# Kernel tuning notes

Measured on AMD Instinct MI355X. Metric: run time of the kernel, lower is better.

Reference implementation:

```python
import jax, jax.numpy as jnp
import numpy as np

H = 64            # hidden_channels
L = 2             # num_layers
E = 300_000       # edges per relation
B = 64            # graphs in batch
NS = [100_000, 20_000, 50_000, 80_000]   # variable, value, operator, constraint
# (src_type, dst_type) for the 9 hetero relations, fixed order
RELS = [(0,1),(0,2),(0,3),(2,3),(3,3),(1,0),(2,0),(3,0),(3,2)]
R = len(RELS)
SLOPE = 0.2       # GATConv leaky_relu negative slope


def setup_inputs() -> dict:
    key = jax.random.key(0)
    ks = iter(jax.random.split(key, 64))
    inp = {}
    for n, N in zip(["x_variable", "x_value", "x_operator", "x_constraint"], NS):
        inp[n] = jax.random.normal(next(ks), (N, H), jnp.float32)
    sc = 1.0 / np.sqrt(H).astype(np.float32)
    inp["Wsrc"] = jax.random.normal(next(ks), (L, R, H, H), jnp.float32) * sc
    inp["Wdst"] = jax.random.normal(next(ks), (L, R, H, H), jnp.float32) * sc
    inp["asrc"] = jax.random.normal(next(ks), (L, R, H), jnp.float32) * sc
    inp["adst"] = jax.random.normal(next(ks), (L, R, H), jnp.float32) * sc
    inp["bias"] = jax.random.normal(next(ks), (L, R, H), jnp.float32) * 0.01
    inp["lin_w"] = jax.random.normal(next(ks), (2, 2 * H), jnp.float32) / np.sqrt(2.0 * H).astype(np.float32)
    inp["lin_b"] = jnp.zeros((2,), jnp.float32)
    for r, (s, d) in enumerate(RELS):
        inp[f"src{r}"] = jax.random.randint(next(ks), (E,), 0, NS[s], jnp.int32)
        inp[f"dst{r}"] = jax.random.randint(next(ks), (E,), 0, NS[d], jnp.int32)
    inp["batch_variable"] = jnp.sort(jax.random.randint(next(ks), (NS[0],), 0, B, jnp.int32))
    inp["batch_constraint"] = jnp.sort(jax.random.randint(next(ks), (NS[3],), 0, B, jnp.int32))
    inp["num_graphs"] = B
    return inp


def _gat(xs, xd, Ws, Wd, a_s, a_d, b, src, dst):
    """Bipartite PyG GATConv (heads=1, add_self_loops=False)."""
    hs = xs @ Ws                         # [Ns, H]
    hd = xd @ Wd                         # [Nd, H]
    al_s = hs @ a_s                      # [Ns]
    al_d = hd @ a_d                      # [Nd]
    score = jax.nn.leaky_relu(al_s[src] + al_d[dst], SLOPE)    # [E]
    nd = xd.shape[0]
    m = jax.ops.segment_max(score, dst, num_segments=nd)
    p = jnp.exp(score - m[dst])
    z = jax.ops.segment_sum(p, dst, num_segments=nd)
    alpha = p / (z[dst] + 1e-16)                               # segment softmax
    out = jax.ops.segment_sum(hs[src] * alpha[:, None], dst, num_segments=nd)
    return out + b


def _seg_mean(x, seg, n):
    s = jax.ops.segment_sum(x, seg, num_segments=n)
    c = jax.ops.segment_sum(jnp.ones((x.shape[0],), x.dtype), seg, num_segments=n)
    return s / jnp.maximum(c, 1.0)[:, None]


def reference(x_variable, x_value, x_operator, x_constraint,
              Wsrc, Wdst, asrc, adst, bias, lin_w, lin_b,
              src0, dst0, src1, dst1, src2, dst2, src3, dst3, src4, dst4,
              src5, dst5, src6, dst6, src7, dst7, src8, dst8,
              batch_variable, batch_constraint, num_graphs):
    xs = [x_variable, x_value, x_operator, x_constraint]
    srcs = [src0, src1, src2, src3, src4, src5, src6, src7, src8]
    dsts = [dst0, dst1, dst2, dst3, dst4, dst5, dst6, dst7, dst8]
    for l in range(L):
        out = [jnp.zeros((x.shape[0], H), x.dtype) for x in xs]
        for r, (s, d) in enumerate(RELS):
            out[d] = out[d] + _gat(xs[s], xs[d], Wsrc[l, r], Wdst[l, r],
                                   asrc[l, r], adst[l, r], bias[l, r],
                                   srcs[r], dsts[r])
        xs = [jax.nn.relu(o) for o in out]   # dropout is identity in eval
    vp = _seg_mean(xs[0], batch_variable, num_graphs)   # [B, H]
    cp = _seg_mean(xs[3], batch_constraint, num_graphs) # [B, H]
    return jnp.concatenate([vp, cp], axis=1) @ lin_w.T + lin_b   # [B, 2]
```

## Files before the change

### kernel.cpp

```cpp
#include <hip/hip_runtime.h>
#include <hip/hip_bf16.h>

#define NH 64
#define NRELS 9
#define NEDGE 300000
#define NGRAPH 64
#define TOTROWS 250000
#define TOTFSEG 660000
#define TOTEDGE (NRELS * NEDGE)
#define NBUCK 977
#define NBC 4
#define CHUNK 2048
#define NBLK ((TOTEDGE + CHUNK - 1) / CHUNK)
#define KCH 20
#define KSP 66
#define BKT_CAP 6144

typedef __attribute__((ext_vector_type(8))) short short8;
typedef __attribute__((ext_vector_type(4))) float f32x4;

__constant__ int c_NS[4]     = {100000, 20000, 50000, 80000};
__constant__ int c_SRC[9]    = {0,0,0,2,3,1,2,3,3};
__constant__ int c_DST[9]    = {1,2,3,3,3,0,0,0,2};
__constant__ int c_XOFF[5]   = {0,100000,120000,170000,250000};
__constant__ int c_ASOFF[10] = {0,100000,200000,300000,350000,430000,450000,500000,580000,660000};
__constant__ int c_FOFF[5]   = {0,300000,320000,420000,660000};
__constant__ int c_NRELT[4]  = {3,1,2,3};
__constant__ int c_RRANK[9]  = {0,0,0,1,2,0,1,2,1};

struct EdgePtrs { const int* s[9]; const int* d[9]; };

__device__ __forceinline__ unsigned short f2bf(float f) {
  union { __hip_bfloat16 h; unsigned short u; } c;
  c.h = __float2bfloat16(f);
  return c.u;
}

__device__ __forceinline__ float wred_max32(float v) {
#pragma unroll
  for (int o = 16; o; o >>= 1) v = fmaxf(v, __shfl_xor(v, o, 32));
  return v;
}

__global__ void k_setup(const float* Wsrc, const float* Wdst, const float* asrc,
                        const float* adst, const float* bias, float* wv, float* bsum) {
  int b = blockIdx.x, j = threadIdx.x;
  if (b < 36) {
    int r = b % 9, q = b / 9;
    int l = q >> 1, side = q & 1;
    const float* W = (side ? Wdst : Wsrc) + (l * 9 + r) * 64 * 64;
    const float* a = (side ? adst : asrc) + (l * 9 + r) * 64;
    float s = 0.f;
    for (int i = 0; i < 64; ++i) s += W[j * 64 + i] * a[i];
    wv[(side ? 1152 : 0) + (l * 9 + r) * 64 + j] = s;
  } else {
    for (int l = 0; l < 2; ++l)
      for (int t = 0; t < 4; ++t) {
        float s = 0.f;
        for (int r = 0; r < 9; ++r)
          if (c_DST[r] == t) s += bias[(l * 9 + r) * 64 + j];
        bsum[(l * 4 + t) * 64 + j] = s;
      }
  }
}

__global__ __launch_bounds__(256) void k_bhist2(EdgePtrs Eg, int* bh) {
  __shared__ int sh[NBUCK];
  for (int i = threadIdx.x; i < NBUCK; i += 256) sh[i] = 0;
  __syncthreads();
  int lo = blockIdx.x * CHUNK;
  int hi = lo + CHUNK; if (hi > TOTEDGE) hi = TOTEDGE;
  for (int gid = lo + threadIdx.x; gid < hi; gid += 256) {
    int r = gid / NEDGE, e = gid - r * NEDGE;
    int g = c_XOFF[c_DST[r]] + Eg.d[r][e];
    atomicAdd(&sh[g >> 8], 1);
  }
  __syncthreads();
  int* dst = bh + (size_t)blockIdx.x * NBUCK;
  for (int i = threadIdx.x; i < NBUCK; i += 256) dst[i] = sh[i];
}

__global__ void k_cs1(const int* bh, int* csum) {
  int blk = blockIdx.x;
  int c = blk / NBC;
  int b = (blk % NBC) * 256 + threadIdx.x;
  if (b >= NBUCK) return;
  int k0 = c * KSP;
  int k1 = k0 + KSP; if (k1 > NBLK) k1 = NBLK;
  int s = 0;
  for (int k = k0; k < k1; ++k) s += bh[(size_t)k * NBUCK + b];
  csum[(size_t)c * NBUCK + b] = s;
}

__global__ void k_cs2(int* csum, int* gbh) {
  int b = blockIdx.x * 256 + threadIdx.x;
  if (b >= NBUCK) return;
  int run = 0;
#pragma unroll
  for (int c = 0; c < KCH; ++c) {
    size_t idx = (size_t)c * NBUCK + b;
    int t = csum[idx];
    csum[idx] = run;
    run += t;
  }
  gbh[b] = run;
}

__global__ void k_cs3(int* bh, const int* csum) {
  int blk = blockIdx.x;
  int c = blk / NBC;
  int b = (blk % NBC) * 256 + threadIdx.x;
  if (b >= NBUCK) return;
  int k0 = c * KSP;
  int k1 = k0 + KSP; if (k1 > NBLK) k1 = NBLK;
  int run = csum[(size_t)c * NBUCK + b];
  for (int k = k0; k < k1; ++k) {
    size_t idx = (size_t)k * NBUCK + b;
    int t = bh[idx];
    bh[idx] = run;
    run += t;
  }
}

__global__ void k_bscan(const int* gbh, int* boff) {
  __shared__ int sd[1024];
  int t = threadIdx.x;
  int v = (t < NBUCK) ? gbh[t] : 0;
  sd[t] = v; __syncthreads();
  for (int o = 1; o < 1024; o <<= 1) {
    int x = (t >= o) ? sd[t - o] : 0; __syncthreads();
    sd[t] += x; __syncthreads();
  }
  if (t < NBUCK) boff[t] = sd[t] - v;
  if (t == 1023) boff[NBUCK] = sd[1023];
}

__global__ __launch_bounds__(256) void k_bin2(EdgePtrs Eg, const int* bh, const int* boff, int* pairs) {
  __shared__ int cur[NBUCK];
  const int* mybh = bh + (size_t)blockIdx.x * NBUCK;
  for (int i = threadIdx.x; i < NBUCK; i += 256) cur[i] = boff[i] + mybh[i];
  __syncthreads();
  int lo = blockIdx.x * CHUNK;
  int hi = lo + CHUNK; if (hi > TOTEDGE) hi = TOTEDGE;
  for (int gid = lo + threadIdx.x; gid < hi; gid += 256) {
    int r = gid / NEDGE, e = gid - r * NEDGE;
    int g = c_XOFF[c_DST[r]] + Eg.d[r][e];
    int b = g >> 8;
    int pos = atomicAdd(&cur[b], 1);
    int key = ((g & 255) << 2) | c_RRANK[r];
    pairs[pos] = (key << 20) | (c_ASOFF[r] + Eg.s[r][e]);
  }
}

__global__ __launch_bounds__(256) void k_bsort(const int* pairs, const int* boff,
                                               int* rowptr, int* asx) {
  __shared__ int spl[BKT_CAP];
  __shared__ int sout[BKT_CAP];
  __shared__ int ssc[1024];
  __shared__ int scur[1024];
  __shared__ int sws[256];
  int b = blockIdx.x, t = threadIdx.x;
  int lo = boff[b], hi = boff[b + 1];
  int n = hi - lo; if (n > BKT_CAP) n = BKT_CAP;
  for (int i = t; i < n; i += 256) spl[i] = pairs[lo + i];
  for (int i = t; i < 1024; i += 256) ssc[i] = 0;
  __syncthreads();
  for (int i = t; i < n; i += 256) atomicAdd(&ssc[((unsigned)spl[i]) >> 20], 1);
  __syncthreads();
  int c0 = ssc[t * 4], c1 = ssc[t * 4 + 1], c2 = ssc[t * 4 + 2], c3 = ssc[t * 4 + 3];
  int s = c0 + c1 + c2 + c3;
  sws[t] = s;
  __syncthreads();
  for (int o = 1; o < 256; o <<= 1) {
    int x = (t >= o) ? sws[t - o] : 0; __syncthreads();
    sws[t] += x; __syncthreads();
  }
  int base = sws[t] - s;
  ssc[t * 4]     = base;
  ssc[t * 4 + 1] = base + c0;
  ssc[t * 4 + 2] = base + c0 + c1;
  ssc[t * 4 + 3] = base + c0 + c1 + c2;
  scur[t * 4]     = ssc[t * 4];
  scur[t * 4 + 1] = ssc[t * 4 + 1];
  scur[t * 4 + 2] = ssc[t * 4 + 2];
  scur[t * 4 + 3] = ssc[t * 4 + 3];
  __syncthreads();
  int nodeBase = b << 8;
  for (int i = t; i < 1024; i += 256) {
    int l = i >> 2, rank = i & 3;
    int g = nodeBase + l;
    if (g < TOTROWS) {
      int tt = (g >= c_XOFF[1]) + (g >= c_XOFF[2]) + (g >= c_XOFF[3]);
      int nr = c_NRELT[tt];
      if (rank < nr)
        rowptr[c_FOFF[tt] + (g - c_XOFF[tt]) * nr + rank] = lo + ssc[i];
    }
  }
  if (b == 0 && t == 0) rowptr[TOTFSEG] = TOTEDGE;
  for (int i = t; i < n; i += 256) {
    int p = spl[i];
    int pos = atomicAdd(&scur[((unsigned)p) >> 20], 1);
    sout[pos] = (int)(((((unsigned)p >> 20) & 3u) << 20) | ((unsigned)p & 0xFFFFFu));
  }
  __syncthreads();
  for (int i = t; i < n; i += 256) asx[lo + i] = sout[i];
}

struct AlphaP {
  const float* x0; const float* x1; const float* x2; const float* x3;
  float* als; float* ald;
  const float* wvs; const float* wvd;
  int act; int smask; int dmask;
};

__global__ __launch_bounds__(256) void k_alphas(AlphaP P) {
  __shared__ float sws[576];
  __shared__ float swd[576];
  for (int i = threadIdx.x; i < 576; i += 256) { sws[i] = P.wvs[i]; swd[i] = P.wvd[i]; }
  __syncthreads();
  int node = blockIdx.x * 256 + threadIdx.x;
  if (node >= TOTROWS) return;
  int t = (node >= c_XOFF[1]) + (node >= c_XOFF[2]) + (node >= c_XOFF[3]);
  int n = node - c_XOFF[t];
  const float* xt = t == 0 ? P.x0 : t == 1 ? P.x1 : t == 2 ? P.x2 : P.x3;
  const float4* rp = (const float4*)xt + (size_t)n * 16;
  float4 row[16];
#pragma unroll
  for (int k = 0; k < 16; ++k) row[k] = rp[k];
  if (P.act) {
#pragma unroll
    for (int k = 0; k < 16; ++k) {
      row[k].x = fmaxf(row[k].x, 0.f); row[k].y = fmaxf(row[k].y, 0.f);
      row[k].z = fmaxf(row[k].z, 0.f); row[k].w = fmaxf(row[k].w, 0.f);
    }
  }
#pragma unroll
  for (int r = 0; r < 9; ++r) {
    bool ns = ((P.smask >> r) & 1) && (c_SRC[r] == t);
    bool nd = ((P.dmask >> r) & 1) && (c_DST[r] == t);
    if (ns) {
      float s = 0.f;
#pragma unroll
      for (int k = 0; k < 16; ++k) {
        float4 w = *(const float4*)&sws[r * 64 + k * 4];
        s += row[k].x * w.x + row[k].y * w.y + row[k].z * w.z + row[k].w * w.w;
      }
      P.als[c_ASOFF[r] + n] = s;
    }
    if (nd) {
      float s = 0.f;
#pragma unroll
      for (int k = 0; k < 16; ++k) {
        float4 w = *(const float4*)&swd[r * 64 + k * 4];
        s += row[k].x * w.x + row[k].y * w.y + row[k].z * w.z + row[k].w * w.w;
      }
      P.ald[c_FOFF[t] + n * c_NRELT[t] + c_RRANK[r]] = s;
    }
  }
}

struct GemmAllP {
  const float* x0; const float* x1; const float* x2; const float* x3;
  const float* Wl;
  __hip_bfloat16* hs;
  int act; int ntyp;
  int tbase[5];
  int typ[4];
  int nrel[4];
  int rel[4][3];
};

#define XSTR 72

__global__ __launch_bounds__(256) void k_gemma(GemmAllP G) {
  __shared__ unsigned short sx[64 * XSTR];
  __shared__ unsigned short sw[64 * XSTR];
  int bid = blockIdx.x;
  int k = 0;
#pragma unroll 3
  for (int q = 1; q < 4; ++q) if (q < G.ntyp) k += (bid >= G.tbase[q]);
  int st = G.typ[k];
  int tile = bid - G.tbase[k];
  int Ns = c_NS[st];
  const float* x = st == 0 ? G.x0 : st == 1 ? G.x1 : st == 2 ? G.x2 : G.x3;
  int base = tile * 64;
  int tid = threadIdx.x;
  for (int kk = tid; kk < 1024; kk += 256) {
    int row = kk >> 4;
    int c4 = (kk & 15) * 4;
    int gr = base + row;
    float4 v = make_float4(0.f, 0.f, 0.f, 0.f);
    if (gr < Ns) v = ((const float4*)x)[(size_t)gr * 16 + (kk & 15)];
    if (G.act) { v.x = fmaxf(v.x, 0.f); v.y = fmaxf(v.y, 0.f); v.z = fmaxf(v.z, 0.f); v.w = fmaxf(v.w, 0.f); }
    ushort4 u;
    u.x = f2bf(v.x); u.y = f2bf(v.y); u.z = f2bf(v.z); u.w = f2bf(v.w);
    *(ushort4*)&sx[row * XSTR + c4] = u;
  }
  __syncthreads();
  int w    = tid >> 6;
  int lane = tid & 63;
  int m    = lane & 15;
  int quad = lane >> 4;
  short8 a0 = *(const short8*)&sx[(w * 16 + m) * XSTR + quad * 8];
  short8 a1 = *(const short8*)&sx[(w * 16 + m) * XSTR + 32 + quad * 8];
  int nrl = G.nrel[k];
  for (int ri = 0; ri < nrl; ++ri) {
    int r = G.rel[k][ri];
    const float* W = G.Wl + r * 4096;
    if (ri) __syncthreads();
    for (int kk = tid; kk < 1024; kk += 256) {
      int krow = kk >> 4;
      int c4 = (kk & 15) * 4;
      float4 v = ((const float4*)W)[kk];
      sw[(c4 + 0) * XSTR + krow] = f2bf(v.x);
      sw[(c4 + 1) * XSTR + krow] = f2bf(v.y);
      sw[(c4 + 2) * XSTR + krow] = f2bf(v.z);
      sw[(c4 + 3) * XSTR + krow] = f2bf(v.w);
    }
    __syncthreads();
    f32x4 acc[4];
#pragma unroll
    for (int cb = 0; cb < 4; ++cb) acc[cb] = (f32x4)(0.f);
#pragma unroll
    for (int cb = 0; cb < 4; ++cb) {
      short8 b0 = *(const short8*)&sw[(cb * 16 + m) * XSTR + quad * 8];
      short8 b1 = *(const short8*)&sw[(cb * 16 + m) * XSTR + 32 + quad * 8];
      acc[cb] = __builtin_amdgcn_mfma_f32_16x16x32_bf16(a0, b0, acc[cb], 0, 0, 0);
      acc[cb] = __builtin_amdgcn_mfma_f32_16x16x32_bf16(a1, b1, acc[cb], 0, 0, 0);
    }
    __hip_bfloat16* hsb = G.hs + (size_t)c_ASOFF[r] * 64;
#pragma unroll
    for (int reg = 0; reg < 4; ++reg) {
      int lr = base + w * 16 + quad * 4 + reg;
      if (lr < Ns) {
#pragma unroll
        for (int cb = 0; cb < 4; ++cb)
          hsb[(size_t)lr * 64 + cb * 16 + m] = __float2bfloat16(acc[cb][reg]);
      }
    }
  }
}

struct GatherAllP {
  const __hip_bfloat16* hs;
  const float* als;
  const float* ald;
  const int* rowptr; const int* asx;
  float* xA;
  const float* bsum;
  int ntypes;
  int tbase[5];
  int typ[4];
};

__global__ __launch_bounds__(256) void k_gatherall(GatherAllP A) {
  __shared__ unsigned long long sRA[8][96];
  __shared__ float sZ[8][4];
  int bid = blockIdx.x;
  int k = 0;
#pragma unroll 3
  for (int q = 1; q < 4; ++q) if (q < A.ntypes) k += (bid >= A.tbase[q]);
  int t = A.typ[k];
  int Nd = c_NS[t];
  int lane = threadIdx.x & 63;
  int half = lane >> 5;
  int sl   = lane & 31;
  int hid  = threadIdx.x >> 5;
  int node = (bid - A.tbase[k]) * 8 + (threadIdx.x >> 6) * 2 + half;
  if (node >= Nd) return;
  int nr = c_NRELT[t];
  int fb = c_FOFF[t] + node * nr;
  int p0 = A.rowptr[fb];
  int p1 = A.rowptr[fb + nr];
  int deg = p1 - p0; if (deg > 96) deg = 96;
  float2 acc = ((const float2*)(A.bsum + t * 64))[sl];
  if (deg > 0) {
    if (sl < 4) sZ[hid][sl] = 0.f;
    const float NEG = -3.4e38f;
    const unsigned* ax = (const unsigned*)A.asx;
    unsigned rec0 = 0, rec1 = 0, rec2 = 0;
    int rk0 = 0, rk1 = 0, rk2 = 0;
    float s0 = NEG, s1 = NEG, s2 = NEG;
    if (sl < deg) {
      rec0 = ax[p0 + sl];
      rk0 = (int)((rec0 >> 20) & 3u);
      float v = A.als[rec0 & 0xFFFFFu] + A.ald[fb + rk0];
      s0 = v >= 0.f ? v : 0.2f * v;
    }
    if (sl + 32 < deg) {
      rec1 = ax[p0 + 32 + sl];
      rk1 = (int)((rec1 >> 20) & 3u);
      float v = A.als[rec1 & 0xFFFFFu] + A.ald[fb + rk1];
      s1 = v >= 0.f ? v : 0.2f * v;
    }
    if (sl + 64 < deg) {
      rec2 = ax[p0 + 64 + sl];
      rk2 = (int)((rec2 >> 20) & 3u);
      float v = A.als[rec2 & 0xFFFFFu] + A.ald[fb + rk2];
      s2 = v >= 0.f ? v : 0.2f * v;
    }
    float M = wred_max32(fmaxf(fmaxf(s0, s1), s2));
    float e0 = 0.f, e1 = 0.f, e2 = 0.f;
    if (sl < deg)      { e0 = __expf(s0 - M); atomicAdd(&sZ[hid][rk0], e0); }
    if (sl + 32 < deg) { e1 = __expf(s1 - M); atomicAdd(&sZ[hid][rk1], e1); }
    if (sl + 64 < deg) { e2 = __expf(s2 - M); atomicAdd(&sZ[hid][rk2], e2); }
    asm volatile("s_waitcnt lgkmcnt(0)" ::: "memory");
    float rz0 = 1.f / (sZ[hid][0] + 1e-16f);
    float rz1 = 1.f / (sZ[hid][1] + 1e-16f);
    float rz2 = 1.f / (sZ[hid][2] + 1e-16f);
    float a0 = e0 * (rk0 == 0 ? rz0 : (rk0 == 1 ? rz1 : rz2));
    sRA[hid][sl] = ((unsigned long long)__float_as_uint(a0) << 32) | ((rec0 & 0xFFFFFu) << 7);
    if (deg > 32) {
      float a1 = e1 * (rk1 == 0 ? rz0 : (rk1 == 1 ? rz1 : rz2));
      sRA[hid][32 + sl] = ((unsigned long long)__float_as_uint(a1) << 32) | ((rec1 & 0xFFFFFu) << 7);
    }
    if (deg > 64) {
      float a2 = e2 * (rk2 == 0 ? rz0 : (rk2 == 1 ? rz1 : rz2));
      sRA[hid][64 + sl] = ((unsigned long long)__float_as_uint(a2) << 32) | ((rec2 & 0xFFFFFu) << 7);
    }
    const char* hsb = (const char*)A.hs;
    unsigned sl4 = (unsigned)sl * 4u;
    int nb = (deg + 7) >> 3;
    for (int g = 0; g < nb; g += 2) {
      unsigned long long raA[8], raB[8];
      unsigned hA[8], hB[8];
      bool hasB = (g + 1) < nb;
#pragma unroll
      for (int q = 0; q < 8; ++q) raA[q] = sRA[hid][g * 8 + q];
#pragma unroll
      for (int q = 0; q < 8; ++q)
        hA[q] = *(const unsigned*)(hsb + ((unsigned)(raA[q] & 0xFFFFFFFFu) + sl4));
      if (hasB) {
#pragma unroll
        for (int q = 0; q < 8; ++q) raB[q] = sRA[hid][g * 8 + 8 + q];
#pragma unroll
        for (int q = 0; q < 8; ++q)
          hB[q] = *(const unsigned*)(hsb + ((unsigned)(raB[q] & 0xFFFFFFFFu) + sl4));
      }
#pragma unroll
      for (int q = 0; q < 8; ++q) {
        float aq = __uint_as_float((unsigned)(raA[q] >> 32));
        acc.x = fmaf(aq, __uint_as_float(hA[q] << 16), acc.x);
        acc.y = fmaf(aq, __uint_as_float(hA[q] & 0xffff0000u), acc.y);
      }
      if (hasB) {
#pragma unroll
        for (int q = 0; q < 8; ++q) {
          float aq = __uint_as_float((unsigned)(raB[q] >> 32));
          acc.x = fmaf(aq, __uint_as_float(hB[q] << 16), acc.x);
          acc.y = fmaf(aq, __uint_as_float(hB[q] & 0xffff0000u), acc.y);
        }
      }
    }
  }
  float* xout = A.xA + (size_t)c_XOFF[t] * 64;
  *(float2*)&xout[(size_t)node * 64 + sl * 2] = acc;
}

__global__ void k_gbound(const int* bvar, const int* bcon, int* gs0, int* gs3) {
  int gid = blockIdx.x * 256 + threadIdx.x;
  const int N0 = 100000, N3 = 80000;
  if (gid < N0) {
    int i = gid;
    int b = bvar[i];
    int bp = i ? bvar[i - 1] : -1;
    for (int g = bp + 1; g <= b; ++g) gs0[g] = i;
    if (i == N0 - 1) for (int g = b + 1; g <= 64; ++g) gs0[g] = N0;
  } else if (gid < N0 + N3) {
    int i = gid - N0;
    int b = bcon[i];
    int bp = i ? bcon[i - 1] : -1;
    for (int g = bp + 1; g <= b; ++g) gs3[g] = i;
    if (i == N3 - 1) for (int g = b + 1; g <= 64; ++g) gs3[g] = N3;
  }
}

__global__ __launch_bounds__(256) void k_pool2(const float* xfin, const int* gs0, const int* gs3,
                                               float* partial) {
  __shared__ float4 sdv[256];
  int b = blockIdx.x;
  int sp = b >> 7;
  int rem = b & 127;
  int g = rem >> 1;
  int t = rem & 1;
  const int* gs = t ? gs3 : gs0;
  int xbase = t ? 170000 : 0;
  int lo = gs[g], hi = gs[g + 1];
  int len = hi - lo;
  int r0 = lo + (len * sp) / 8;
  int r1 = lo + (len * (sp + 1)) / 8;
  int tid = threadIdx.x;
  int rp = tid >> 4;
  int cq = tid & 15;
  float4 acc = make_float4(0.f, 0.f, 0.f, 0.f);
  for (int row = r0 + rp; row < r1; row += 16) {
    float4 v = ((const float4*)xfin)[(size_t)(xbase + row) * 16 + cq];
    acc.x += fmaxf(v.x, 0.f); acc.y += fmaxf(v.y, 0.f);
    acc.z += fmaxf(v.z, 0.f); acc.w += fmaxf(v.w, 0.f);
  }
  sdv[tid] = acc;
  __syncthreads();
  for (int o = 128; o >= 16; o >>= 1) {
    if (tid < o) {
      float4 a = sdv[tid], c = sdv[tid + o];
      a.x += c.x; a.y += c.y; a.z += c.z; a.w += c.w;
      sdv[tid] = a;
    }
    __syncthreads();
  }
  if (tid < 16) ((float4*)&partial[(size_t)b * 64])[tid] = sdv[tid];
}

__global__ void k_poolred2(const float* partial, float* pool) {
  int g = blockIdx.x >> 1;
  int t = blockIdx.x & 1;
  int col = threadIdx.x;
  float s = 0.f;
#pragma unroll
  for (int sp = 0; sp < 8; ++sp)
    s += partial[(size_t)(((sp << 7) | (g << 1) | t)) * 64 + col];
  pool[(t ? 4096 : 0) + g * 64 + col] = s;
}

__global__ void k_final(const float* pool, const int* gs0, const int* gs3,
                        const float* lin_w, const float* lin_b, float* out) {
  int k = threadIdx.x;
  int g = k >> 1, o = k & 1;
  float c0 = fmaxf((float)(gs0[g + 1] - gs0[g]), 1.f);
  float c3 = fmaxf((float)(gs3[g + 1] - gs3[g]), 1.f);
  float acc = lin_b[o];
  for (int i = 0; i < 64; ++i) {
    acc += (pool[g * 64 + i] / c0) * lin_w[o * 128 + i];
    acc += (pool[4096 + g * 64 + i] / c3) * lin_w[o * 128 + 64 + i];
  }
  out[g * 2 + o] = acc;
}

__global__ void k_bail(float* out) {
  if (threadIdx.x < 128) out[threadIdx.x] = 0.f;
}

extern "C" void kernel_launch(void* const* d_in, const int* in_sizes, int n_in,
                              void* d_out, int out_size, void* d_ws, size_t ws_size,
                              hipStream_t stream) {
  (void)in_sizes; (void)n_in; (void)out_size;
  const size_t O_XA   = 0;
  const size_t O_HS   = 16000000;
  const size_t O_ALS  = 37120000;
  const size_t O_ALD  = 37780000;
  const size_t O_WV   = 39790000;
  const size_t O_BS   = 39792304;
  const size_t O_RP   = 39792816;
  const size_t O_ASX  = 40452832;
  const size_t O_GS   = 43152832;
  const size_t O_PART = 43153088;
  const size_t O_POOL = 43218624;
  const size_t NEED   = 43226816;

  if (ws_size < NEED * 4) {
    k_bail<<<1, 128, 0, stream>>>((float*)d_out);
    return;
  }

  const float* x0 = (const float*)d_in[0];
  const float* x1 = (const float*)d_in[1];
  const float* x2 = (const float*)d_in[2];
  const float* x3 = (const float*)d_in[3];
  const float* Wsrc = (const float*)d_in[4];
  const float* Wdst = (const float*)d_in[5];
  const float* asrc = (const float*)d_in[6];
  const float* adst = (const float*)d_in[7];
  const float* bias = (const float*)d_in[8];
  const float* lin_w = (const float*)d_in[9];
  const float* lin_b = (const float*)d_in[10];
  EdgePtrs Eg;
  for (int r = 0; r < 9; ++r) {
    Eg.s[r] = (const int*)d_in[11 + 2 * r];
    Eg.d[r] = (const int*)d_in[12 + 2 * r];
  }
  const int* bvar = (const int*)d_in[29];
  const int* bcon = (const int*)d_in[30];

  float* ws = (float*)d_ws;
  float* xA   = ws + O_XA;
  __hip_bfloat16* hs = (__hip_bfloat16*)(ws + O_HS);
  int* bh     = (int*)(ws + O_HS);
  int* pairs  = bh + (size_t)NBLK * NBUCK;
  int* gbh    = pairs + 2700000;
  int* boff   = gbh + (NBUCK + 1);
  int* csum   = boff + (NBUCK + 2);
  float* als  = ws + O_ALS;
  float* ald  = ws + O_ALD;
  float* wv   = ws + O_WV;
  float* bsum = ws + O_BS;
  int* rowptr = (int*)(ws + O_RP);
  int* asx    = (int*)(ws + O_ASX);
  int* gs0    = (int*)(ws + O_GS);
  int* gs3    = gs0 + 65;
  float* partial = ws + O_PART;
  float* pool = ws + O_POOL;

  const int h_NS[4]   = {100000, 20000, 50000, 80000};
  const int h_SRC[9]  = {0,0,0,2,3,1,2,3,3};
  const int h_XOFF[4] = {0,100000,120000,170000};

  k_setup<<<37, 64, 0, stream>>>(Wsrc, Wdst, asrc, adst, bias, wv, bsum);

  k_bhist2<<<NBLK, 256, 0, stream>>>(Eg, bh);
  k_cs1<<<KCH * NBC, 256, 0, stream>>>(bh, csum);
  k_cs2<<<NBC, 256, 0, stream>>>(csum, gbh);
  k_cs3<<<KCH * NBC, 256, 0, stream>>>(bh, csum);
  k_bscan<<<1, 1024, 0, stream>>>(gbh, boff);
  k_bin2<<<NBLK, 256, 0, stream>>>(Eg, bh, boff, pairs);
  k_bsort<<<NBUCK, 256, 0, stream>>>(pairs, boff, rowptr, asx);
  k_gbound<<<(180000 + 255) / 256, 256, 0, stream>>>(bvar, bcon, gs0, gs3);

  for (int l = 0; l < 2; ++l) {
    const float* xin[4];
    if (l == 0) { xin[0] = x0; xin[1] = x1; xin[2] = x2; xin[3] = x3; }
    else {
      for (int t = 0; t < 4; ++t) xin[t] = xA + (size_t)h_XOFF[t] * 64;
    }
    int act = (l > 0);
    int relmask = l ? 0x0FC : 0x1FF;

    AlphaP AP;
    AP.x0 = xin[0]; AP.x1 = xin[1]; AP.x2 = xin[2]; AP.x3 = xin[3];
    AP.als = als; AP.ald = ald;
    AP.wvs = wv + l * 576; AP.wvd = wv + 1152 + l * 576;
    AP.act = act; AP.smask = relmask; AP.dmask = relmask;
    k_alphas<<<(TOTROWS + 255) / 256, 256, 0, stream>>>(AP);

    GemmAllP G;
    G.x0 = xin[0]; G.x1 = xin[1]; G.x2 = xin[2]; G.x3 = xin[3];
    G.Wl = Wsrc + (size_t)l * 9 * 4096;
    G.hs = hs; G.act = act;
    int ntyp = 0, cum = 0;
    for (int t = 0; t < 4; ++t) {
      int nr = 0; int rl[3];
      for (int r = 0; r < 9; ++r)
        if (((relmask >> r) & 1) && h_SRC[r] == t) rl[nr++] = r;
      if (!nr) continue;
      G.typ[ntyp] = t; G.nrel[ntyp] = nr;
      for (int i = 0; i < 3; ++i) G.rel[ntyp][i] = (i < nr) ? rl[i] : 0;
      G.tbase[ntyp] = cum;
      cum += (h_NS[t] + 63) / 64;
      ++ntyp;
    }
    G.ntyp = ntyp; G.tbase[ntyp] = cum;
    k_gemma<<<cum, 256, 0, stream>>>(G);

    GatherAllP A;
    A.hs = hs; A.als = als; A.ald = ald;
    A.rowptr = rowptr; A.asx = asx;
    A.xA = xA;
    A.bsum = bsum + l * 256;
    int nt = 0, bcum = 0;
    for (int t = 0; t < 4; ++t) {
      if (l == 1 && (t == 1 || t == 2)) continue;
      A.typ[nt] = t;
      A.tbase[nt] = bcum;
      bcum += (h_NS[t] + 7) / 8;
      ++nt;
    }
    A.ntypes = nt; A.tbase[nt] = bcum;
    k_gatherall<<<bcum, 256, 0, stream>>>(A);
  }

  k_pool2<<<1024, 256, 0, stream>>>(xA, gs0, gs3, partial);
  k_poolred2<<<128, 64, 0, stream>>>(partial, pool);
  k_final<<<1, 128, 0, stream>>>(pool, gs0, gs3, lin_w, lin_b, (float*)d_out);
}
```

Before: 504.1 us.

## Fuse attention-logit computation into GEMM kernel and pre-convert weights to bf16

Removes the separate k_alphas kernel and computes per-node source and destination attention logits inside k_gemma, reusing the x tile rows each block already reads. Source weights are transposed and converted to bf16 once in k_setup, so each GEMM block copies them with vector loads instead of converting and scattering in shared memory. The change also doubles the edge chunk size for histogram and binning (halving KSP to match) and precomputes the softmax reciprocals once per segment in shared memory. The fused kernel now also covers node types that are only destinations, and it rereads x rows from global memory and reads the wv vectors directly from global memory rather than from shared memory.

```diff
diff --git a/kernel.cpp b/kernel.cpp
--- a/kernel.cpp
+++ b/kernel.cpp
@@ -10,10 +10,10 @@
 #define TOTEDGE (NRELS * NEDGE)
 #define NBUCK 977
 #define NBC 4
-#define CHUNK 2048
+#define CHUNK 4096
 #define NBLK ((TOTEDGE + CHUNK - 1) / CHUNK)
 #define KCH 20
-#define KSP 66
+#define KSP 33
 #define BKT_CAP 6144
 
 typedef __attribute__((ext_vector_type(8))) short short8;
@@ -43,7 +43,8 @@
 }
 
 __global__ void k_setup(const float* Wsrc, const float* Wdst, const float* asrc,
-                        const float* adst, const float* bias, float* wv, float* bsum) {
+                        const float* adst, const float* bias, float* wv, float* bsum,
+                        unsigned short* wb) {
   int b = blockIdx.x, j = threadIdx.x;
   if (b < 36) {
     int r = b % 9, q = b / 9;
@@ -53,7 +54,7 @@
     float s = 0.f;
     for (int i = 0; i < 64; ++i) s += W[j * 64 + i] * a[i];
     wv[(side ? 1152 : 0) + (l * 9 + r) * 64 + j] = s;
-  } else {
+  } else if (b == 36) {
     for (int l = 0; l < 2; ++l)
       for (int t = 0; t < 4; ++t) {
         float s = 0.f;
@@ -61,6 +62,13 @@
           if (c_DST[r] == t) s += bias[(l * 9 + r) * 64 + j];
         bsum[(l * 4 + t) * 64 + j] = s;
       }
+  } else {
+    int idx = b - 37;
+    int l = idx / 9, r = idx % 9;
+    const float* W = Wsrc + (size_t)(l * 9 + r) * 4096;
+    unsigned short* dst = wb + (size_t)(l * 9 + r) * 4096;
+    for (int k = 0; k < 64; ++k)
+      dst[j * 64 + k] = f2bf(W[k * 64 + j]);
   }
 }
 
@@ -206,68 +214,19 @@
   for (int i = t; i < n; i += 256) asx[lo + i] = sout[i];
 }
 
-struct AlphaP {
+struct GemmAllP {
   const float* x0; const float* x1; const float* x2; const float* x3;
+  const unsigned short* Wb;
+  __hip_bfloat16* hs;
   float* als; float* ald;
   const float* wvs; const float* wvd;
-  int act; int smask; int dmask;
-};
-
-__global__ __launch_bounds__(256) void k_alphas(AlphaP P) {
-  __shared__ float sws[576];
-  __shared__ float swd[576];
-  for (int i = threadIdx.x; i < 576; i += 256) { sws[i] = P.wvs[i]; swd[i] = P.wvd[i]; }
-  __syncthreads();
-  int node = blockIdx.x * 256 + threadIdx.x;
-  if (node >= TOTROWS) return;
-  int t = (node >= c_XOFF[1]) + (node >= c_XOFF[2]) + (node >= c_XOFF[3]);
-  int n = node - c_XOFF[t];
-  const float* xt = t == 0 ? P.x0 : t == 1 ? P.x1 : t == 2 ? P.x2 : P.x3;
-  const float4* rp = (const float4*)xt + (size_t)n * 16;
-  float4 row[16];
-#pragma unroll
-  for (int k = 0; k < 16; ++k) row[k] = rp[k];
-  if (P.act) {
-#pragma unroll
-    for (int k = 0; k < 16; ++k) {
-      row[k].x = fmaxf(row[k].x, 0.f); row[k].y = fmaxf(row[k].y, 0.f);
-      row[k].z = fmaxf(row[k].z, 0.f); row[k].w = fmaxf(row[k].w, 0.f);
-    }
-  }
-#pragma unroll
-  for (int r = 0; r < 9; ++r) {
-    bool ns = ((P.smask >> r) & 1) && (c_SRC[r] == t);
-    bool nd = ((P.dmask >> r) & 1) && (c_DST[r] == t);
-    if (ns) {
-      float s = 0.f;
-#pragma unroll
-      for (int k = 0; k < 16; ++k) {
-        float4 w = *(const float4*)&sws[r * 64 + k * 4];
-        s += row[k].x * w.x + row[k].y * w.y + row[k].z * w.z + row[k].w * w.w;
-      }
-      P.als[c_ASOFF[r] + n] = s;
-    }
-    if (nd) {
-      float s = 0.f;
-#pragma unroll
-      for (int k = 0; k < 16; ++k) {
-        float4 w = *(const float4*)&swd[r * 64 + k * 4];
-        s += row[k].x * w.x + row[k].y * w.y + row[k].z * w.z + row[k].w * w.w;
-      }
-      P.ald[c_FOFF[t] + n * c_NRELT[t] + c_RRANK[r]] = s;
-    }
-  }
-}
-
-struct GemmAllP {
-  const float* x0; const float* x1; const float* x2; const float* x3;
-  const float* Wl;
-  __hip_bfloat16* hs;
   int act; int ntyp;
   int tbase[5];
   int typ[4];
   int nrel[4];
   int rel[4][3];
+  int ndrel[4];
+  int drel[4][3];
 };
 
 #define XSTR 72
@@ -297,6 +256,46 @@
     *(ushort4*)&sx[row * XSTR + c4] = u;
   }
   __syncthreads();
+  {
+    int row = tid >> 2, part = tid & 3;
+    int gr2 = base + row;
+    if (gr2 < Ns) {
+      float xv[16];
+      const float4* xr = (const float4*)x + (size_t)gr2 * 16 + part * 4;
+      float4 v0 = xr[0], v1 = xr[1], v2 = xr[2], v3 = xr[3];
+      xv[0]=v0.x; xv[1]=v0.y; xv[2]=v0.z; xv[3]=v0.w;
+      xv[4]=v1.x; xv[5]=v1.y; xv[6]=v1.z; xv[7]=v1.w;
+      xv[8]=v2.x; xv[9]=v2.y; xv[10]=v2.z; xv[11]=v2.w;
+      xv[12]=v3.x; xv[13]=v3.y; xv[14]=v3.z; xv[15]=v3.w;
+      if (G.act) {
+#pragma unroll
+        for (int i = 0; i < 16; ++i) xv[i] = fmaxf(xv[i], 0.f);
+      }
+      int nrl0 = G.nrel[k];
+      for (int ri = 0; ri < nrl0; ++ri) {
+        int r = G.rel[k][ri];
+        const float* wvp = G.wvs + r * 64 + part * 16;
+        float s = 0.f;
+#pragma unroll
+        for (int i = 0; i < 16; ++i) s += xv[i] * wvp[i];
+        s += __shfl_xor(s, 1);
+        s += __shfl_xor(s, 2);
+        if (part == 0) G.als[c_ASOFF[r] + gr2] = s;
+      }
+      int ndl = G.ndrel[k];
+      for (int ri = 0; ri < ndl; ++ri) {
+        int r = G.drel[k][ri];
+        const float* wvp = G.wvd + r * 64 + part * 16;
+        float s = 0.f;
+#pragma unroll
+        for (int i = 0; i < 16; ++i) s += xv[i] * wvp[i];
+        s += __shfl_xor(s, 1);
+        s += __shfl_xor(s, 2);
+        if (part == 0)
+          G.ald[c_FOFF[st] + gr2 * c_NRELT[st] + c_RRANK[r]] = s;
+      }
+    }
+  }
   int w    = tid >> 6;
   int lane = tid & 63;
   int m    = lane & 15;
@@ -306,16 +305,15 @@
   int nrl = G.nrel[k];
   for (int ri = 0; ri < nrl; ++ri) {
     int r = G.rel[k][ri];
-    const float* W = G.Wl + r * 4096;
+    const unsigned short* Wb = G.Wb + (size_t)r * 4096;
     if (ri) __syncthreads();
-    for (int kk = tid; kk < 1024; kk += 256) {
-      int krow = kk >> 4;
-      int c4 = (kk & 15) * 4;
-      float4 v = ((const float4*)W)[kk];
-      sw[(c4 + 0) * XSTR + krow] = f2bf(v.x);
-      sw[(c4 + 1) * XSTR + krow] = f2bf(v.y);
-      sw[(c4 + 2) * XSTR + krow] = f2bf(v.z);
-      sw[(c4 + 3) * XSTR + krow] = f2bf(v.w);
+    {
+      int n = tid >> 2;
+      int k0 = (tid & 3) << 4;
+      short8 w0 = *(const short8*)&Wb[n * 64 + k0];
+      short8 w1 = *(const short8*)&Wb[n * 64 + k0 + 8];
+      *(short8*)&sw[n * XSTR + k0] = w0;
+      *(short8*)&sw[n * XSTR + k0 + 8] = w1;
     }
     __syncthreads();
     f32x4 acc[4];
@@ -405,17 +403,16 @@
     if (sl + 32 < deg) { e1 = __expf(s1 - M); atomicAdd(&sZ[hid][rk1], e1); }
     if (sl + 64 < deg) { e2 = __expf(s2 - M); atomicAdd(&sZ[hid][rk2], e2); }
     asm volatile("s_waitcnt lgkmcnt(0)" ::: "memory");
-    float rz0 = 1.f / (sZ[hid][0] + 1e-16f);
-    float rz1 = 1.f / (sZ[hid][1] + 1e-16f);
-    float rz2 = 1.f / (sZ[hid][2] + 1e-16f);
-    float a0 = e0 * (rk0 == 0 ? rz0 : (rk0 == 1 ? rz1 : rz2));
+    if (sl < 3) { float z = sZ[hid][sl]; sZ[hid][sl] = 1.f / (z + 1e-16f); }
+    asm volatile("s_waitcnt lgkmcnt(0)" ::: "memory");
+    float a0 = e0 * sZ[hid][rk0];
     sRA[hid][sl] = ((unsigned long long)__float_as_uint(a0) << 32) | ((rec0 & 0xFFFFFu) << 7);
     if (deg > 32) {
-      float a1 = e1 * (rk1 == 0 ? rz0 : (rk1 == 1 ? rz1 : rz2));
+      float a1 = e1 * sZ[hid][rk1];
       sRA[hid][32 + sl] = ((unsigned long long)__float_as_uint(a1) << 32) | ((rec1 & 0xFFFFFu) << 7);
     }
     if (deg > 64) {
-      float a2 = e2 * (rk2 == 0 ? rz0 : (rk2 == 1 ? rz1 : rz2));
+      float a2 = e2 * sZ[hid][rk2];
       sRA[hid][64 + sl] = ((unsigned long long)__float_as_uint(a2) << 32) | ((rec2 & 0xFFFFFu) << 7);
     }
     const char* hsb = (const char*)A.hs;
@@ -555,7 +552,8 @@
   const size_t O_GS   = 43152832;
   const size_t O_PART = 43153088;
   const size_t O_POOL = 43218624;
-  const size_t NEED   = 43226816;
+  const size_t O_WB   = 43226816;
+  const size_t NEED   = 43263680;
 
   if (ws_size < NEED * 4) {
     k_bail<<<1, 128, 0, stream>>>((float*)d_out);
@@ -599,12 +597,14 @@
   int* gs3    = gs0 + 65;
   float* partial = ws + O_PART;
   float* pool = ws + O_POOL;
+  unsigned short* wb = (unsigned short*)(ws + O_WB);
 
   const int h_NS[4]   = {100000, 20000, 50000, 80000};
   const int h_SRC[9]  = {0,0,0,2,3,1,2,3,3};
+  const int h_DST[9]  = {1,2,3,3,3,0,0,0,2};
   const int h_XOFF[4] = {0,100000,120000,170000};
 
-  k_setup<<<37, 64, 0, stream>>>(Wsrc, Wdst, asrc, adst, bias, wv, bsum);
+  k_setup<<<55, 64, 0, stream>>>(Wsrc, Wdst, asrc, adst, bias, wv, bsum, wb);
 
   k_bhist2<<<NBLK, 256, 0, stream>>>(Eg, bh);
   k_cs1<<<KCH * NBC, 256, 0, stream>>>(bh, csum);
@@ -624,25 +624,26 @@
     int act = (l > 0);
     int relmask = l ? 0x0FC : 0x1FF;
 
-    AlphaP AP;
-    AP.x0 = xin[0]; AP.x1 = xin[1]; AP.x2 = xin[2]; AP.x3 = xin[3];
-    AP.als = als; AP.ald = ald;
-    AP.wvs = wv + l * 576; AP.wvd = wv + 1152 + l * 576;
-    AP.act = act; AP.smask = relmask; AP.dmask = relmask;
-    k_alphas<<<(TOTROWS + 255) / 256, 256, 0, stream>>>(AP);
-
     GemmAllP G;
     G.x0 = xin[0]; G.x1 = xin[1]; G.x2 = xin[2]; G.x3 = xin[3];
-    G.Wl = Wsrc + (size_t)l * 9 * 4096;
+    G.Wb = wb + (size_t)l * 9 * 4096;
     G.hs = hs; G.act = act;
+    G.als = als; G.ald = ald;
+    G.wvs = wv + l * 576; G.wvd = wv + 1152 + l * 576;
     int ntyp = 0, cum = 0;
     for (int t = 0; t < 4; ++t) {
-      int nr = 0; int rl[3];
-      for (int r = 0; r < 9; ++r)
-        if (((relmask >> r) & 1) && h_SRC[r] == t) rl[nr++] = r;
-      if (!nr) continue;
-      G.typ[ntyp] = t; G.nrel[ntyp] = nr;
-      for (int i = 0; i < 3; ++i) G.rel[ntyp][i] = (i < nr) ? rl[i] : 0;
+      int nr = 0; int rl[3]; int nd = 0; int dl[3];
+      for (int r = 0; r < 9; ++r) {
+        if (!((relmask >> r) & 1)) continue;
+        if (h_SRC[r] == t) rl[nr++] = r;
+        if (h_DST[r] == t) dl[nd++] = r;
+      }
+      if (!nr && !nd) continue;
+      G.typ[ntyp] = t; G.nrel[ntyp] = nr; G.ndrel[ntyp] = nd;
+      for (int i = 0; i < 3; ++i) {
+        G.rel[ntyp][i]  = (i < nr) ? rl[i] : 0;
+        G.drel[ntyp][i] = (i < nd) ? dl[i] : 0;
+      }
       G.tbase[ntyp] = cum;
       cum += (h_NS[t] + 63) / 64;
       ++ntyp;
```

Result: faster. 492.5 us (-2.3%).
